# Kernel optimization log

Hardware: AMD Instinct MI355X
Metric: run time of the kernel (lower is better)

## Reference

```python
import jax, jax.numpy as jnp
import numpy as np
import math

N = 50000      # nodes
E = 800000     # edges
D = 128        # in/out channels (hidden_dim)
H = 16         # heads
C = D // H     # per-head channels = 8
DH = 4 * D     # mlp hidden = 512
EPS = 1e-5


def layernorm(x, g, b):
    mu = jnp.mean(x, axis=-1, keepdims=True)
    var = jnp.var(x, axis=-1, keepdims=True)
    return (x - mu) * jax.lax.rsqrt(var + EPS) * g + b


def setup_inputs() -> dict:
    key = jax.random.key(0)
    ks = jax.random.split(key, 16)
    s = lambda k, shape, fan: jax.random.normal(k, shape, jnp.float32) / np.sqrt(fan)
    inp = {
        "x": jax.random.normal(ks[0], (N, D), jnp.float32),
        "edge_index": jax.random.randint(ks[1], (2, E), 0, N, jnp.int32),
        "edge_attr": jax.random.normal(ks[2], (E, D), jnp.float32),
        # layer norm 1
        "ln1_g": jnp.ones((D,), jnp.float32), "ln1_b": jnp.zeros((D,), jnp.float32),
        # q/k/v/self projections (in=D, out=H*C=D)
        "wq": s(ks[3], (D, D), D), "bq": jnp.zeros((D,), jnp.float32),
        "wk": s(ks[4], (D, D), D), "bk": jnp.zeros((D,), jnp.float32),
        "wv": s(ks[5], (D, D), D), "bv": jnp.zeros((D,), jnp.float32),
        "ws": s(ks[6], (D, D), D), "bs": jnp.zeros((D,), jnp.float32),
        # edge projection (edge_dim=D -> H*C)
        "we": s(ks[7], (D, D), D), "be": jnp.zeros((D,), jnp.float32),
        # output projection
        "wp": s(ks[8], (D, D), D), "bp": jnp.zeros((D,), jnp.float32),
        # node_dst_mlp: LN -> Linear(D,4D) -> SiLU -> Linear(4D,D)
        "mlp_ln_g": jnp.ones((D,), jnp.float32), "mlp_ln_b": jnp.zeros((D,), jnp.float32),
        "w1": s(ks[9], (D, DH), D), "b1": jnp.zeros((DH,), jnp.float32),
        "w2": s(ks[10], (DH, D), DH), "b2": jnp.zeros((D,), jnp.float32),
    }
    return inp


def reference(x, edge_index, edge_attr, ln1_g, ln1_b, wq, bq, wk, bk, wv, bv,
              ws, bs, we, be, wp, bp, mlp_ln_g, mlp_ln_b, w1, b1, w2, b2):
    src, dst = edge_index[0], edge_index[1]  # message j -> i

    h = layernorm(x, ln1_g, ln1_b)
    q = (h @ wq + bq).reshape(N, H, C)
    k = (h @ wk + bk).reshape(N, H, C)
    v = (h @ wv + bv).reshape(N, H, C)
    x_r = h @ ws + bs                         # [N, D]

    # per-edge gather + edge-feature add
    k_j = k[src] + (edge_attr @ we + be).reshape(E, H, C)  # [E,H,C]
    alpha = jnp.sum(q[dst] * k_j, axis=-1) / math.sqrt(C)  # [E,H]

    # segment softmax over destination nodes
    m = jax.ops.segment_max(alpha, dst, num_segments=N)    # [N,H]
    ex = jnp.exp(alpha - m[dst])
    denom = jax.ops.segment_sum(ex, dst, num_segments=N)   # [N,H]
    alpha = ex / denom[dst]

    # weighted scatter-add aggregation
    msg = v[src] * alpha[..., None]                        # [E,H,C]
    agg = jax.ops.segment_sum(msg, dst, num_segments=N).reshape(N, D)

    out = (agg + x_r) @ wp + bp
    out = out + x                                          # residual to raw input
    mlp_out = jax.nn.silu(layernorm(out, mlp_ln_g, mlp_ln_b) @ w1 + b1) @ w2 + b2
    return mlp_out + out
```

## Files before the change

### kernel.cpp

```cpp
#include <hip/hip_runtime.h>

#define N_NODES 50000
#define N_EDGES 800000
#define D 128
#define H 16
#define DH 512

typedef __attribute__((ext_vector_type(8))) short short8;
typedef __attribute__((ext_vector_type(4))) float f32x4;

static __device__ __forceinline__ unsigned short f2bf(float f) {
    unsigned u = __float_as_uint(f);
    u += 0x7FFF + ((u >> 16) & 1);
    return (unsigned short)(u >> 16);
}
static __device__ __forceinline__ float bf2f(unsigned short u) {
    return __uint_as_float(((unsigned)u) << 16);
}

__global__ void ln_kernel(const float* __restrict__ x, const float* __restrict__ g,
                          const float* __restrict__ b, unsigned short* __restrict__ out, int n) {
    int w = (blockIdx.x * blockDim.x + threadIdx.x) >> 6;
    int lane = threadIdx.x & 63;
    if (w >= n) return;
    float2 v = *(const float2*)(x + (size_t)w * D + lane * 2);
    float s = v.x + v.y, ss = v.x * v.x + v.y * v.y;
#pragma unroll
    for (int off = 32; off; off >>= 1) { s += __shfl_xor(s, off); ss += __shfl_xor(ss, off); }
    float mean = s * (1.0f / D);
    float var = ss * (1.0f / D) - mean * mean;
    float rstd = rsqrtf(var + 1e-5f);
    float2 gv = *(const float2*)(g + lane * 2);
    float2 bv = *(const float2*)(b + lane * 2);
    ushort2 o;
    o.x = f2bf((v.x - mean) * rstd * gv.x + bv.x);
    o.y = f2bf((v.y - mean) * rstd * gv.y + bv.y);
    *(ushort2*)(out + (size_t)w * D + lane * 2) = o;
}

__global__ void prep_kernel(const float* __restrict__ wq, const float* __restrict__ wk,
                            const float* __restrict__ wv, const float* __restrict__ ws,
                            const float* __restrict__ we, const float* __restrict__ wp,
                            const float* __restrict__ w1, const float* __restrict__ w2,
                            const float* __restrict__ bq, const float* __restrict__ bk,
                            const float* __restrict__ bv, const float* __restrict__ bs,
                            unsigned short* __restrict__ wqkvsT, unsigned short* __restrict__ weT,
                            unsigned short* __restrict__ wpT, unsigned short* __restrict__ w1T,
                            unsigned short* __restrict__ w2T, float* __restrict__ bias_qkvs) {
    int idx = blockIdx.x * blockDim.x + threadIdx.x;
    if (idx < 65536) {
        int seg = idx >> 14, r = idx & 16383;
        const float* src = seg == 0 ? wq : seg == 1 ? wk : seg == 2 ? wv : ws;
        int o = r >> 7, i = r & 127;
        wqkvsT[idx] = f2bf(src[i * 128 + o]);
    } else if (idx < 81920) {
        int r = idx - 65536; int o = r >> 7, i = r & 127;
        weT[r] = f2bf(we[i * 128 + o]);
    } else if (idx < 98304) {
        int r = idx - 81920; int o = r >> 7, i = r & 127;
        wpT[r] = f2bf(wp[i * 128 + o]);
    } else if (idx < 163840) {
        int r = idx - 98304; int o = r >> 7, i = r & 127;
        w1T[r] = f2bf(w1[i * 512 + o]);
    } else if (idx < 229376) {
        int r = idx - 163840; int o = r >> 9, i = r & 511;
        w2T[r] = f2bf(w2[i * 128 + o]);
    } else if (idx < 229888) {
        int r = idx - 229376;
        const float* p = r < 128 ? bq : r < 256 ? bk : r < 384 ? bv : bs;
        bias_qkvs[r] = p[r & 127];
    }
}

__global__ void hist_kernel(const int* __restrict__ edge_index, int* __restrict__ counts) {
    int e = blockIdx.x * blockDim.x + threadIdx.x;
    if (e < N_EDGES) atomicAdd(&counts[edge_index[N_EDGES + e]], 1);
}

__global__ void scan1_kernel(const int* __restrict__ counts, int* __restrict__ excl,
                             int* __restrict__ bsum) {
    __shared__ int sm[1024];
    int b = blockIdx.x, tid = threadIdx.x;
    int idx = b * 1024 + tid;
    int v = (idx < N_NODES) ? counts[idx] : 0;
    sm[tid] = v;
    __syncthreads();
    for (int off = 1; off < 1024; off <<= 1) {
        int t = (tid >= off) ? sm[tid - off] : 0;
        __syncthreads();
        sm[tid] += t;
        __syncthreads();
    }
    if (idx < N_NODES) excl[idx] = sm[tid] - v;
    if (tid == 1023) bsum[b] = sm[1023];
}

__global__ void scan2_kernel(int* __restrict__ bsum, int nb) {
    if (threadIdx.x == 0 && blockIdx.x == 0) {
        int run = 0;
        for (int i = 0; i < nb; ++i) { int v = bsum[i]; bsum[i] = run; run += v; }
    }
}

__global__ void scan3_kernel(const int* __restrict__ excl, const int* __restrict__ bsum,
                             int* __restrict__ row_ptr, int* __restrict__ cursor) {
    int b = blockIdx.x, tid = threadIdx.x;
    int idx = b * 1024 + tid;
    if (idx < N_NODES) {
        int v = bsum[b] + excl[idx];
        row_ptr[idx] = v;
        cursor[idx] = v;
    }
    if (idx == 0) row_ptr[N_NODES] = N_EDGES;
}

__global__ void scatter_kernel(const int* __restrict__ edge_index, int* __restrict__ cursor,
                               int* __restrict__ slot_of, int* __restrict__ src_ord) {
    int e = blockIdx.x * blockDim.x + threadIdx.x;
    if (e < N_EDGES) {
        int dst = edge_index[N_EDGES + e];
        int pos = atomicAdd(&cursor[dst], 1);
        slot_of[e] = pos;
        src_ord[pos] = edge_index[e];
    }
}

enum { EPI_F32 = 0, EPI_RESID = 1, EPI_SILU_BF = 2, EPI_ADDOUT = 3, EPI_BF16 = 4 };

template <int KD, int EPI>
__global__ void gemm_kernel(const unsigned short* __restrict__ A, const unsigned short* __restrict__ BT,
                            const float* __restrict__ bias, void* __restrict__ outp,
                            const float* __restrict__ extra, int M, int Nout) {
    int wave = threadIdx.x >> 6, lane = threadIdx.x & 63;
    int lr = lane & 15, lq = lane >> 4;
    int row0 = (blockIdx.x * 4 + wave) * 16;
    int col0 = blockIdx.y * 64;
    int arow = row0 + lr;
    if (arow >= M) arow = M - 1;
    f32x4 z = {0.f, 0.f, 0.f, 0.f};
    f32x4 acc[4] = {z, z, z, z};
#pragma unroll
    for (int t = 0; t < KD / 32; ++t) {
        short8 a = *(const short8*)(A + (size_t)arow * KD + t * 32 + lq * 8);
#pragma unroll
        for (int cf = 0; cf < 4; ++cf) {
            short8 b = *(const short8*)(BT + (size_t)(col0 + cf * 16 + lr) * KD + t * 32 + lq * 8);
            acc[cf] = __builtin_amdgcn_mfma_f32_16x16x32_bf16(a, b, acc[cf], 0, 0, 0);
        }
    }
#pragma unroll
    for (int cf = 0; cf < 4; ++cf) {
        int col = col0 + cf * 16 + lr;
        float bv = bias[col];
#pragma unroll
        for (int r = 0; r < 4; ++r) {
            int row = row0 + lq * 4 + r;
            if (row >= M) continue;
            float v = acc[cf][r] + bv;
            if (EPI == EPI_F32) {
                ((float*)outp)[(size_t)row * Nout + col] = v;
            } else if (EPI == EPI_RESID) {
                ((float*)outp)[(size_t)row * Nout + col] = v + extra[(size_t)row * D + col];
            } else if (EPI == EPI_SILU_BF) {
                float sg = 1.0f / (1.0f + __expf(-v));
                ((unsigned short*)outp)[(size_t)row * Nout + col] = f2bf(v * sg);
            } else if (EPI == EPI_ADDOUT) {
                ((float*)outp)[(size_t)row * Nout + col] = v + extra[(size_t)row * D + col];
            } else {
                ((unsigned short*)outp)[(size_t)row * Nout + col] = f2bf(v);
            }
        }
    }
}

#define ES_GRID 3584
__global__ __launch_bounds__(128)
void edge_score_kernel(const float* __restrict__ edge_attr,
                       const unsigned short* __restrict__ weT,
                       const float* __restrict__ be, const int* __restrict__ edge_index,
                       const int* __restrict__ slot_of,
                       const unsigned short* __restrict__ qkvs,
                       float* __restrict__ qE) {
    __shared__ unsigned short q_lds[32][132];
    __shared__ float s_lds[32][20];
    const int NTILE = N_EDGES / 32;
    int wave = threadIdx.x >> 6, lane = threadIdx.x & 63;
    int lr = lane & 15, lq = lane >> 4;
    int w16 = wave * 16;
    int plane = lane >> 5, h2 = lane & 31;

    for (int tile = blockIdx.x; tile < NTILE; tile += ES_GRID) {
        int e0w = tile * 32 + w16;

        f32x4 lo[4], hi[4];
#pragma unroll
        for (int t = 0; t < 4; ++t) {
            const f32x4* p = (const f32x4*)(edge_attr + (size_t)(e0w + lr) * D + t * 32 + lq * 8);
            lo[t] = __builtin_nontemporal_load(p);
            hi[t] = __builtin_nontemporal_load(p + 1);
        }

        int dstv = edge_index[N_EDGES + e0w + lr];
        int slotv = slot_of[e0w + lr];
        ushort4 qreg[8];
#pragma unroll
        for (int it = 0; it < 8; ++it) {
            int dst = __shfl(dstv, it * 2 + plane);
            qreg[it] = *(const ushort4*)(qkvs + (size_t)dst * 512 + h2 * 4);
        }

        short8 a[4];
#pragma unroll
        for (int t = 0; t < 4; ++t) {
            short8 av;
            av[0] = f2bf(lo[t][0]); av[1] = f2bf(lo[t][1]); av[2] = f2bf(lo[t][2]); av[3] = f2bf(lo[t][3]);
            av[4] = f2bf(hi[t][0]); av[5] = f2bf(hi[t][1]); av[6] = f2bf(hi[t][2]); av[7] = f2bf(hi[t][3]);
            a[t] = av;
        }

#pragma unroll
        for (int it = 0; it < 8; ++it)
            *(ushort4*)(&q_lds[w16 + it * 2 + plane][h2 * 4]) = qreg[it];

        f32x4 z = {0.f, 0.f, 0.f, 0.f};
        f32x4 acc[8] = {z, z, z, z, z, z, z, z};
#pragma unroll
        for (int cf = 0; cf < 8; ++cf) {
#pragma unroll
            for (int t = 0; t < 4; ++t) {
                short8 b = *(const short8*)(weT + (size_t)(cf * 16 + lr) * D + t * 32 + lq * 8);
                acc[cf] = __builtin_amdgcn_mfma_f32_16x16x32_bf16(b, a[t], acc[cf], 0, 0, 0);
            }
        }

#pragma unroll
        for (int cf = 0; cf < 8; ++cf) {
            int ch = cf * 16 + lq * 4;
            ushort4 q4 = *(const ushort4*)(&q_lds[w16 + lr][ch]);
            f32x4 be4 = *(const f32x4*)(be + ch);
            float p = bf2f(q4.x) * (acc[cf][0] + be4[0])
                    + bf2f(q4.y) * (acc[cf][1] + be4[1])
                    + bf2f(q4.z) * (acc[cf][2] + be4[2])
                    + bf2f(q4.w) * (acc[cf][3] + be4[3]);
            p += __shfl_xor(p, 16);
            if ((lq & 1) == 0)
                s_lds[w16 + lr][cf * 2 + (lq >> 1)] = p;
        }

        int el16 = lane >> 2;
        int slot = __shfl(slotv, el16);
        f32x4 sv = *(const f32x4*)(&s_lds[w16 + el16][(lane & 3) * 4]);
        *(f32x4*)(qE + (size_t)slot * 16 + (lane & 3) * 4) = sv;
    }
}

__global__ void agg_kernel(const int* __restrict__ row_ptr, const int* __restrict__ src_ord,
                           const float* __restrict__ qE, const unsigned short* __restrict__ qkvs,
                           unsigned short* __restrict__ aggxr) {
    int w = (blockIdx.x * blockDim.x + threadIdx.x) >> 6;
    int lane = threadIdx.x & 63;
    if (w >= N_NODES) return;
    int c = lane * 2, h = lane >> 2;
    int s = row_ptr[w], e = row_ptr[w + 1], deg = e - s;
    int src_p = (lane < deg) ? src_ord[s + lane] : 0;
    ushort2 q2 = *(const ushort2*)(qkvs + (size_t)w * 512 + c);
    float qa = bf2f(q2.x), qb = bf2f(q2.y);
    const float scale = 0.35355339059327373f;
    float acc0 = 0.f, acc1 = 0.f, den = 0.f;
    for (int i = 0; i < deg; ++i) {
        int src = (i < 64) ? __shfl(src_p, i) : src_ord[s + i];
        ushort2 k2 = *(const ushort2*)(qkvs + (size_t)src * 512 + 128 + c);
        ushort2 v2 = *(const ushort2*)(qkvs + (size_t)src * 512 + 256 + c);
        float pa = qa * bf2f(k2.x) + qb * bf2f(k2.y);
        pa += __shfl_xor(pa, 1);
        pa += __shfl_xor(pa, 2);
        float qEv = qE[(size_t)(s + i) * 16 + h];
        float ex = __expf((pa + qEv) * scale);
        acc0 += ex * bf2f(v2.x);
        acc1 += ex * bf2f(v2.y);
        den += ex;
    }
    float inv = den > 0.f ? 1.0f / den : 0.f;
    ushort2 x2 = *(const ushort2*)(qkvs + (size_t)w * 512 + 384 + c);
    ushort2 o;
    o.x = f2bf(acc0 * inv + bf2f(x2.x));
    o.y = f2bf(acc1 * inv + bf2f(x2.y));
    *(ushort2*)(aggxr + (size_t)w * D + c) = o;
}

extern "C" void kernel_launch(void* const* d_in, const int* in_sizes, int n_in,
                              void* d_out, int out_size, void* d_ws, size_t ws_size,
                              hipStream_t stream) {
    const float* x = (const float*)d_in[0];
    const int* edge_index = (const int*)d_in[1];
    const float* edge_attr = (const float*)d_in[2];
    const float* ln1_g = (const float*)d_in[3];
    const float* ln1_b = (const float*)d_in[4];
    const float* wq = (const float*)d_in[5];  const float* bq = (const float*)d_in[6];
    const float* wk = (const float*)d_in[7];  const float* bk = (const float*)d_in[8];
    const float* wv = (const float*)d_in[9];  const float* bv = (const float*)d_in[10];
    const float* wsw = (const float*)d_in[11]; const float* bs = (const float*)d_in[12];
    const float* we = (const float*)d_in[13]; const float* be = (const float*)d_in[14];
    const float* wp = (const float*)d_in[15]; const float* bp = (const float*)d_in[16];
    const float* mlp_g = (const float*)d_in[17]; const float* mlp_b = (const float*)d_in[18];
    const float* w1 = (const float*)d_in[19]; const float* b1 = (const float*)d_in[20];
    const float* w2 = (const float*)d_in[21]; const float* b2 = (const float*)d_in[22];

    char* base = (char*)d_ws;
    size_t off = 0;
    auto alloc = [&](size_t bytes) -> char* {
        char* p = base + off;
        off = (off + bytes + 255) & ~(size_t)255;
        return p;
    };
    unsigned short* qkvs   = (unsigned short*)alloc((size_t)N_NODES * 512 * 2);
    float* qE_buf          = (float*)alloc((size_t)N_EDGES * H * 4);
    unsigned short* h_bf   = (unsigned short*)alloc((size_t)N_NODES * D * 2);
    unsigned short* aggxr  = (unsigned short*)alloc((size_t)N_NODES * D * 2);
    float* outbuf          = (float*)alloc((size_t)N_NODES * D * 4);
    unsigned short* ln2_bf = (unsigned short*)alloc((size_t)N_NODES * D * 2);
    unsigned short* silu_bf= (unsigned short*)alloc((size_t)N_NODES * DH * 2);
    int* counts            = (int*)alloc((size_t)N_NODES * 4);
    int* row_ptr           = (int*)alloc((size_t)(N_NODES + 1) * 4);
    int* cursor            = (int*)alloc((size_t)N_NODES * 4);
    int* slot_of           = (int*)alloc((size_t)N_EDGES * 4);
    int* src_ord           = (int*)alloc((size_t)N_EDGES * 4);
    int* excl              = (int*)alloc((size_t)N_NODES * 4);
    int* bsum              = (int*)alloc(64 * 4);
    unsigned short* wqkvsT = (unsigned short*)alloc(512 * 128 * 2);
    unsigned short* weT    = (unsigned short*)alloc(128 * 128 * 2);
    unsigned short* wpT    = (unsigned short*)alloc(128 * 128 * 2);
    unsigned short* w1T    = (unsigned short*)alloc(512 * 128 * 2);
    unsigned short* w2T    = (unsigned short*)alloc(128 * 512 * 2);
    float* bias_qkvs       = (float*)alloc(512 * 4);

    const int NB = (N_NODES + 1023) / 1024;

    prep_kernel<<<898, 256, 0, stream>>>(wq, wk, wv, wsw, we, wp, w1, w2, bq, bk, bv, bs,
                                         wqkvsT, weT, wpT, w1T, w2T, bias_qkvs);

    (void)hipMemsetAsync(counts, 0, (size_t)N_NODES * 4, stream);
    hist_kernel<<<(N_EDGES + 255) / 256, 256, 0, stream>>>(edge_index, counts);
    scan1_kernel<<<NB, 1024, 0, stream>>>(counts, excl, bsum);
    scan2_kernel<<<1, 64, 0, stream>>>(bsum, NB);
    scan3_kernel<<<NB, 1024, 0, stream>>>(excl, bsum, row_ptr, cursor);
    scatter_kernel<<<(N_EDGES + 255) / 256, 256, 0, stream>>>(edge_index, cursor, slot_of, src_ord);

    ln_kernel<<<(N_NODES + 3) / 4, 256, 0, stream>>>(x, ln1_g, ln1_b, h_bf, N_NODES);

    dim3 g_node((N_NODES + 63) / 64, 8);
    gemm_kernel<128, EPI_BF16><<<g_node, 256, 0, stream>>>(h_bf, wqkvsT, bias_qkvs, qkvs, nullptr, N_NODES, 512);

    edge_score_kernel<<<ES_GRID, 128, 0, stream>>>(edge_attr, weT, be, edge_index, slot_of, qkvs, qE_buf);

    agg_kernel<<<(N_NODES + 3) / 4, 256, 0, stream>>>(row_ptr, src_ord, qE_buf, qkvs, aggxr);

    dim3 g_out((N_NODES + 63) / 64, 2);
    gemm_kernel<128, EPI_RESID><<<g_out, 256, 0, stream>>>(aggxr, wpT, bp, outbuf, x, N_NODES, 128);

    ln_kernel<<<(N_NODES + 3) / 4, 256, 0, stream>>>(outbuf, mlp_g, mlp_b, ln2_bf, N_NODES);

    dim3 g_mlp1((N_NODES + 63) / 64, 8);
    gemm_kernel<128, EPI_SILU_BF><<<g_mlp1, 256, 0, stream>>>(ln2_bf, w1T, b1, silu_bf, nullptr, N_NODES, 512);

    dim3 g_mlp2((N_NODES + 63) / 64, 2);
    gemm_kernel<512, EPI_ADDOUT><<<g_mlp2, 256, 0, stream>>>(silu_bf, w2T, b2, (float*)d_out, outbuf, N_NODES, 128);
}
```

Measured before the change: 614.0 us.

## Interleave K/V in qkvs, store edge scores as bf16, persistent agg grid

The QKVS GEMM epilogue now writes K and V channels interleaved, so the aggregation loop fetches both with a single 8-byte gather per edge instead of two 4-byte gathers. Per-edge edge-score terms are stored as bf16 rather than fp32, halving that write/read traffic. The aggregation kernel becomes a grid-stride loop with a fixed grid. The risks are reduced precision on the attention logits and scattered 2-byte stores in the GEMM epilogue.

New measurement: 615.4 us, median of 2. About the same (+0.2%).

```diff
diff --git a/kernel.cpp b/kernel.cpp
--- a/kernel.cpp
+++ b/kernel.cpp
@@ -125,7 +125,7 @@
     }
 }
 
-enum { EPI_F32 = 0, EPI_RESID = 1, EPI_SILU_BF = 2, EPI_ADDOUT = 3, EPI_BF16 = 4 };
+enum { EPI_F32 = 0, EPI_RESID = 1, EPI_SILU_BF = 2, EPI_ADDOUT = 3, EPI_BF16 = 4, EPI_QKVS = 5 };
 
 template <int KD, int EPI>
 __global__ void gemm_kernel(const unsigned short* __restrict__ A, const unsigned short* __restrict__ BT,
@@ -166,6 +166,11 @@
                 ((unsigned short*)outp)[(size_t)row * Nout + col] = f2bf(v * sg);
             } else if (EPI == EPI_ADDOUT) {
                 ((float*)outp)[(size_t)row * Nout + col] = v + extra[(size_t)row * D + col];
+            } else if (EPI == EPI_QKVS) {
+                int seg = col >> 7, c = col & 127;
+                size_t o = (seg == 0) ? (size_t)c : (seg == 1) ? (size_t)(128 + 2 * c)
+                         : (seg == 2) ? (size_t)(129 + 2 * c) : (size_t)(384 + c);
+                ((unsigned short*)outp)[(size_t)row * 512 + o] = f2bf(v);
             } else {
                 ((unsigned short*)outp)[(size_t)row * Nout + col] = f2bf(v);
             }
@@ -180,7 +185,7 @@
                        const float* __restrict__ be, const int* __restrict__ edge_index,
                        const int* __restrict__ slot_of,
                        const unsigned short* __restrict__ qkvs,
-                       float* __restrict__ qE) {
+                       unsigned short* __restrict__ qE16) {
     __shared__ unsigned short q_lds[32][132];
     __shared__ float s_lds[32][20];
     const int NTILE = N_EDGES / 32;
@@ -250,42 +255,45 @@
         int el16 = lane >> 2;
         int slot = __shfl(slotv, el16);
         f32x4 sv = *(const f32x4*)(&s_lds[w16 + el16][(lane & 3) * 4]);
-        *(f32x4*)(qE + (size_t)slot * 16 + (lane & 3) * 4) = sv;
-    }
-}
-
+        ushort4 o;
+        o.x = f2bf(sv[0]); o.y = f2bf(sv[1]); o.z = f2bf(sv[2]); o.w = f2bf(sv[3]);
+        *(ushort4*)(qE16 + (size_t)slot * 16 + (lane & 3) * 4) = o;
+    }
+}
+
+#define AGG_GRID 2048
 __global__ void agg_kernel(const int* __restrict__ row_ptr, const int* __restrict__ src_ord,
-                           const float* __restrict__ qE, const unsigned short* __restrict__ qkvs,
+                           const unsigned short* __restrict__ qE16, const unsigned short* __restrict__ qkvs,
                            unsigned short* __restrict__ aggxr) {
-    int w = (blockIdx.x * blockDim.x + threadIdx.x) >> 6;
     int lane = threadIdx.x & 63;
-    if (w >= N_NODES) return;
     int c = lane * 2, h = lane >> 2;
-    int s = row_ptr[w], e = row_ptr[w + 1], deg = e - s;
-    int src_p = (lane < deg) ? src_ord[s + lane] : 0;
-    ushort2 q2 = *(const ushort2*)(qkvs + (size_t)w * 512 + c);
-    float qa = bf2f(q2.x), qb = bf2f(q2.y);
     const float scale = 0.35355339059327373f;
-    float acc0 = 0.f, acc1 = 0.f, den = 0.f;
-    for (int i = 0; i < deg; ++i) {
-        int src = (i < 64) ? __shfl(src_p, i) : src_ord[s + i];
-        ushort2 k2 = *(const ushort2*)(qkvs + (size_t)src * 512 + 128 + c);
-        ushort2 v2 = *(const ushort2*)(qkvs + (size_t)src * 512 + 256 + c);
-        float pa = qa * bf2f(k2.x) + qb * bf2f(k2.y);
-        pa += __shfl_xor(pa, 1);
-        pa += __shfl_xor(pa, 2);
-        float qEv = qE[(size_t)(s + i) * 16 + h];
-        float ex = __expf((pa + qEv) * scale);
-        acc0 += ex * bf2f(v2.x);
-        acc1 += ex * bf2f(v2.y);
-        den += ex;
-    }
-    float inv = den > 0.f ? 1.0f / den : 0.f;
-    ushort2 x2 = *(const ushort2*)(qkvs + (size_t)w * 512 + 384 + c);
-    ushort2 o;
-    o.x = f2bf(acc0 * inv + bf2f(x2.x));
-    o.y = f2bf(acc1 * inv + bf2f(x2.y));
-    *(ushort2*)(aggxr + (size_t)w * D + c) = o;
+    int nw = (AGG_GRID * 256) >> 6;
+    for (int w = (int)((blockIdx.x * blockDim.x + threadIdx.x) >> 6); w < N_NODES; w += nw) {
+        int s = row_ptr[w], e = row_ptr[w + 1], deg = e - s;
+        int src_p = (lane < deg) ? src_ord[s + lane] : 0;
+        ushort2 q2 = *(const ushort2*)(qkvs + (size_t)w * 512 + c);
+        float qa = bf2f(q2.x), qb = bf2f(q2.y);
+        float acc0 = 0.f, acc1 = 0.f, den = 0.f;
+        for (int i = 0; i < deg; ++i) {
+            int src = (i < 64) ? __shfl(src_p, i) : src_ord[s + i];
+            ushort4 kv = *(const ushort4*)(qkvs + (size_t)src * 512 + 128 + (size_t)c * 2);
+            float pa = qa * bf2f(kv.x) + qb * bf2f(kv.z);
+            pa += __shfl_xor(pa, 1);
+            pa += __shfl_xor(pa, 2);
+            float qEv = bf2f(qE16[(size_t)(s + i) * 16 + h]);
+            float ex = __expf((pa + qEv) * scale);
+            acc0 += ex * bf2f(kv.y);
+            acc1 += ex * bf2f(kv.w);
+            den += ex;
+        }
+        float inv = den > 0.f ? 1.0f / den : 0.f;
+        ushort2 x2 = *(const ushort2*)(qkvs + (size_t)w * 512 + 384 + c);
+        ushort2 o;
+        o.x = f2bf(acc0 * inv + bf2f(x2.x));
+        o.y = f2bf(acc1 * inv + bf2f(x2.y));
+        *(ushort2*)(aggxr + (size_t)w * D + c) = o;
+    }
 }
 
 extern "C" void kernel_launch(void* const* d_in, const int* in_sizes, int n_in,
@@ -314,7 +322,7 @@
         return p;
     };
     unsigned short* qkvs   = (unsigned short*)alloc((size_t)N_NODES * 512 * 2);
-    float* qE_buf          = (float*)alloc((size_t)N_EDGES * H * 4);
+    unsigned short* qE16   = (unsigned short*)alloc((size_t)N_EDGES * H * 2);
     unsigned short* h_bf   = (unsigned short*)alloc((size_t)N_NODES * D * 2);
     unsigned short* aggxr  = (unsigned short*)alloc((size_t)N_NODES * D * 2);
     float* outbuf          = (float*)alloc((size_t)N_NODES * D * 4);
@@ -349,11 +357,11 @@
     ln_kernel<<<(N_NODES + 3) / 4, 256, 0, stream>>>(x, ln1_g, ln1_b, h_bf, N_NODES);
 
     dim3 g_node((N_NODES + 63) / 64, 8);
-    gemm_kernel<128, EPI_BF16><<<g_node, 256, 0, stream>>>(h_bf, wqkvsT, bias_qkvs, qkvs, nullptr, N_NODES, 512);
-
-    edge_score_kernel<<<ES_GRID, 128, 0, stream>>>(edge_attr, weT, be, edge_index, slot_of, qkvs, qE_buf);
-
-    agg_kernel<<<(N_NODES + 3) / 4, 256, 0, stream>>>(row_ptr, src_ord, qE_buf, qkvs, aggxr);
+    gemm_kernel<128, EPI_QKVS><<<g_node, 256, 0, stream>>>(h_bf, wqkvsT, bias_qkvs, qkvs, nullptr, N_NODES, 512);
+
+    edge_score_kernel<<<ES_GRID, 128, 0, stream>>>(edge_attr, weT, be, edge_index, slot_of, qkvs, qE16);
+
+    agg_kernel<<<AGG_GRID, 256, 0, stream>>>(row_ptr, src_ord, qE16, qkvs, aggxr);
 
     dim3 g_out((N_NODES + 63) / 64, 2);
     gemm_kernel<128, EPI_RESID><<<g_out, 256, 0, stream>>>(aggxr, wpT, bp, outbuf, x, N_NODES, 128);
```
